# Performance work log

Hardware: AMD Instinct MI355X
Metric: run time of the kernel (lower is better)

Reference implementation:

```python
import jax, jax.numpy as jnp
import numpy as np

NEG_SLOPE = 0.2
CHUNK = 64  # target-node chunk size to bound the [B,c,N,H,D] intermediate


def layer_norm(x, g, b, eps=1e-5):
    mu = jnp.mean(x, axis=-1, keepdims=True)
    var = jnp.mean((x - mu) ** 2, axis=-1, keepdims=True)
    return (x - mu) / jnp.sqrt(var + eps) * g + b


def gatv2_dense(x, Wl, bl, Wr, br, att, bias):
    """GATv2 (PyG semantics, concat=True) on a fully-connected graph with self-loops.
    x: [B,N,Fin]; att: [H,D]. Returns [B,N,H*D].
    e_ij = att_h . leaky_relu(xl_j + xr_i); softmax over sources j; out_i = sum_j a_ij xl_j.
    """
    B, N, _ = x.shape
    H, D = att.shape
    xl = (x @ Wl + bl).reshape(B, N, H, D)  # source-side (lin_l)
    xr = (x @ Wr + br).reshape(B, N, H, D)  # target-side (lin_r)
    nc = N // CHUNK
    xr_ch = jnp.moveaxis(xr.reshape(B, nc, CHUNK, H, D), 1, 0)  # [nc,B,c,H,D]

    @jax.checkpoint
    def per_chunk(xr_c):  # xr_c: [B,c,H,D]
        z = jax.nn.leaky_relu(xr_c[:, :, None] + xl[:, None], NEG_SLOPE)  # [B,c,N,H,D]
        e = jnp.einsum('bcjhd,hd->bcjh', z, att)
        a = jax.nn.softmax(e, axis=2)  # softmax over sources j
        return jnp.einsum('bcjh,bjhd->bchd', a, xl)

    out = jax.lax.map(per_chunk, xr_ch)  # [nc,B,c,H,D]
    return jnp.moveaxis(out, 0, 1).reshape(B, N, H * D) + bias


def setup_inputs() -> dict:
    key = jax.random.key(0)
    ks = jax.random.split(key, 12)
    B, N, Fin, Hd, H, Do = 4, 2048, 32, 32, 4, 32
    f32 = jnp.float32

    def glorot(k, shape, fan_in):
        return jax.random.normal(k, shape, f32) * (1.0 / np.sqrt(fan_in))

    return {
        'x': jax.random.normal(ks[0], (B, N, Fin), f32),
        'embedding': jax.random.normal(ks[1], (N, Hd), f32),
        # layer 1: in=Fin, heads=H, head dim=Hd
        'Wl1': glorot(ks[2], (Fin, H * Hd), Fin), 'bl1': jnp.zeros((H * Hd,), f32),
        'Wr1': glorot(ks[3], (Fin, H * Hd), Fin), 'br1': jnp.zeros((H * Hd,), f32),
        'att1': glorot(ks[4], (H, Hd), Hd), 'bias1': jnp.zeros((H * Hd,), f32),
        'ln1_g': jnp.ones((H * Hd,), f32), 'ln1_b': jnp.zeros((H * Hd,), f32),
        # layer 2: in=H*Hd, heads=H, head dim=Do
        'Wl2': glorot(ks[5], (H * Hd, H * Do), H * Hd), 'bl2': jnp.zeros((H * Do,), f32),
        'Wr2': glorot(ks[6], (H * Hd, H * Do), H * Hd), 'br2': jnp.zeros((H * Do,), f32),
        'att2': glorot(ks[7], (H, Do), Do), 'bias2': jnp.zeros((H * Do,), f32),
        'ln2_g': jnp.ones((H * Do,), f32), 'ln2_b': jnp.zeros((H * Do,), f32),
    }


def reference(x, embedding, Wl1, bl1, Wr1, br1, att1, bias1, ln1_g, ln1_b,
              Wl2, bl2, Wr2, br2, att2, bias2, ln2_g, ln2_b):
    # AdaptiveAdjacency: cosine-similarity gram matrix. Its values are generically
    # all nonzero, so adj[b].nonzero() yields a fully-connected edge list including
    # self-loops; only the connectivity (dense) is consumed downstream.
    ne = embedding / jnp.linalg.norm(embedding, axis=1, keepdims=True)
    adj = ne @ ne.T  # [N,N]; connectivity only (dense), values unused by GATv2
    del adj

    h = layer_norm(gatv2_dense(x, Wl1, bl1, Wr1, br1, att1, bias1), ln1_g, ln1_b)
    h = jax.nn.relu(h)
    # dropout(p=0.3) is identity in eval mode
    out = layer_norm(gatv2_dense(h, Wl2, bl2, Wr2, br2, att2, bias2), ln2_g, ln2_b)
    return out
```

## Files before the change

kernel.cpp:

```cpp
#include <hip/hip_runtime.h>
#include <math.h>

#define LOG2E 1.4426950408889634f

#if __has_builtin(__builtin_amdgcn_exp2f)
#define EXP2(x) __builtin_amdgcn_exp2f(x)
#else
#define EXP2(x) exp2f(x)
#endif

constexpr int B_ = 4, N_ = 2048, H_ = 4, D_ = 32, HD_ = 128;
constexpr int BH_ = B_ * H_;
constexpr int ROWS_ = BH_ * N_;
constexpr size_t M_ = (size_t)ROWS_ * D_;

typedef float v4f __attribute__((ext_vector_type(4)));
typedef _Float16 h2 __attribute__((ext_vector_type(2)));

static __device__ __forceinline__ h2 habs2(h2 z) {
    unsigned int t = __builtin_bit_cast(unsigned int, z) & 0x7FFF7FFFu;
    return __builtin_bit_cast(h2, t);
}
static __device__ __forceinline__ h2 hadd2u(unsigned int a, unsigned int b) {
    return __builtin_bit_cast(h2, a) + __builtin_bit_cast(h2, b);
}
static __device__ __forceinline__ h2 u2h(unsigned int a) {
    return __builtin_bit_cast(h2, a);
}

__global__ __launch_bounds__(256) void k_linear(
    const float* __restrict__ x,
    const float* __restrict__ Wl, const float* __restrict__ bl,
    const float* __restrict__ Wr, const float* __restrict__ br,
    float* __restrict__ xl, unsigned short* __restrict__ xlh,
    unsigned short* __restrict__ xrh, unsigned int* __restrict__ xlpT, int K)
{
    __shared__ __align__(16) float xs[32 * 128];
    const int tid = threadIdx.x;
    const int r0 = blockIdx.x * 32;
    const float4* src = (const float4*)(x + (size_t)r0 * K);
    float4* dst = (float4*)xs;
    for (int idx = tid; idx < 8 * K; idx += 256) dst[idx] = src[idx];
    __syncthreads();

    const int c  = tid & 127;
    const int rg = tid >> 7;
    float accl[16], accr[16];
    const float blv = bl[c], brv = br[c];
    #pragma unroll
    for (int r = 0; r < 16; r++) { accl[r] = blv; accr[r] = brv; }
    #pragma unroll 8
    for (int k = 0; k < K; k++) {
        const float wl = Wl[k * HD_ + c];
        const float wr = Wr[k * HD_ + c];
        #pragma unroll
        for (int r = 0; r < 16; r++) {
            const float xv = xs[(rg * 16 + r) * K + k];
            accl[r] = fmaf(xv, wl, accl[r]);
            accr[r] = fmaf(xv, wr, accr[r]);
        }
    }
    const int h = c >> 5, d = c & 31;
    #pragma unroll
    for (int r = 0; r < 16; r++) {
        const int row = r0 + rg * 16 + r;
        const int b = row >> 11, n = row & (N_ - 1);
        const size_t o = (((size_t)(b * H_ + h)) * N_ + n) * D_ + d;
        xl[o] = accl[r];
        xlh[o] = __builtin_bit_cast(unsigned short, (_Float16)accl[r]);
        xrh[o] = __builtin_bit_cast(unsigned short, (_Float16)accr[r]);
    }
    #pragma unroll
    for (int r = 0; r < 16; r += 2) {
        const int row = r0 + rg * 16 + r;
        const int b = row >> 11, n = row & (N_ - 1);
        h2 pr;
        pr.x = (_Float16)accl[r];
        pr.y = (_Float16)accl[r + 1];
        const size_t o = (((size_t)(b * H_ + h)) * (N_ / 2) + (n >> 1)) * D_ + d;
        xlpT[o] = __builtin_bit_cast(unsigned int, pr);
    }
}

__global__ __launch_bounds__(256) void k_u(
    const float* __restrict__ xl, const float* __restrict__ att,
    float* __restrict__ u)
{
    const int idx = blockIdx.x * 256 + threadIdx.x;
    const int h = (idx / N_) & (H_ - 1);
    const float4* a4 = (const float4*)(att + h * D_);
    const float4* l4 = (const float4*)(xl + (size_t)idx * D_);
    float su = 0.f;
    #pragma unroll
    for (int q = 0; q < 8; q++) {
        const float4 a = a4[q], lv = l4[q];
        su += a.x * lv.x + a.y * lv.y + a.z * lv.z + a.w * lv.w;
    }
    u[idx] = 0.6f * LOG2E * su;
}

__global__ __launch_bounds__(512) void k_bound(
    const unsigned int* __restrict__ xlh, const unsigned int* __restrict__ xrh,
    const float* __restrict__ u, const float* __restrict__ att,
    float* __restrict__ bound, unsigned int* __restrict__ tch)
{
    __shared__ float redA[16][33];
    __shared__ float redB[16][33];
    __shared__ float clv[32];
    __shared__ float tca[32];
    __shared__ float redu[512];
    const int bh = blockIdx.x, h = bh & (H_ - 1), t = threadIdx.x;

    if (bh < H_ && t < 16) {
        h2 v;
        v.x = (_Float16)(att[bh * D_ + 2 * t]     * (0.4f * LOG2E));
        v.y = (_Float16)(att[bh * D_ + 2 * t + 1] * (0.4f * LOG2E));
        tch[bh * 16 + t] = __builtin_bit_cast(unsigned int, v);
    }
    if (t < 16) {
        _Float16 a = (_Float16)(att[h * D_ + 2 * t]     * (0.4f * LOG2E));
        _Float16 b = (_Float16)(att[h * D_ + 2 * t + 1] * (0.4f * LOG2E));
        tca[2 * t]     = fabsf((float)a);
        tca[2 * t + 1] = fabsf((float)b);
    }
    const unsigned int* xb = xlh + (size_t)bh * N_ * 16;
    const int p = t & 15, rg = t >> 4;
    float m0 = 0.f, m1 = 0.f;
    for (int r = rg; r < N_; r += 32) {
        h2 z = __builtin_bit_cast(h2, xb[r * 16 + p] & 0x7FFF7FFFu);
        m0 = fmaxf(m0, (float)z.x);
        m1 = fmaxf(m1, (float)z.y);
    }
    redA[p][rg] = m0; redB[p][rg] = m1;
    const float* ub = u + (size_t)bh * N_;
    float um = -1e30f;
    for (int r = t; r < N_; r += 512) um = fmaxf(um, ub[r]);
    redu[t] = um;
    __syncthreads();
    if (t < 16) {
        float a = 0.f, b = 0.f;
        for (int g = 0; g < 32; g++) { a = fmaxf(a, redA[t][g]); b = fmaxf(b, redB[t][g]); }
        clv[2 * t] = a; clv[2 * t + 1] = b;
    }
    for (int s = 256; s > 0; s >>= 1) {
        if (t < s) redu[t] = fmaxf(redu[t], redu[t + s]);
        __syncthreads();
    }
    const float umax = redu[0];
    const unsigned int* xrb = xrh + (size_t)bh * N_ * 16;
    for (int r = t; r < N_; r += 512) {
        float s = 0.f;
        #pragma unroll
        for (int k = 0; k < 16; k++) {
            h2 z = __builtin_bit_cast(h2, xrb[r * 16 + k] & 0x7FFF7FFFu);
            s += tca[2 * k] * (clv[2 * k] + (float)z.x)
               + tca[2 * k + 1] * (clv[2 * k + 1] + (float)z.y);
        }
        bound[bh * N_ + r] = umax + s + 0.25f;
    }
}

__global__ __launch_bounds__(256) void k_attn(
    const unsigned int* __restrict__ xlh,
    const unsigned int* __restrict__ xlpT,
    const unsigned int* __restrict__ xrh,
    const float* __restrict__ u, const float* __restrict__ bound,
    const unsigned int* __restrict__ tch,
    float* __restrict__ P, float* __restrict__ lb, int jlen)
{
    const int tid = threadIdx.x, lane = tid & 63, wid = tid >> 6;
    const int t128 = blockIdx.x & 127, part = blockIdx.x >> 7;
    const int bh = t128 >> 3;
    const int h  = bh & (H_ - 1);
    const int row = bh * N_ + (t128 & 7) * 256 + wid * 64 + lane;

    h2 tc[16];
    #pragma unroll
    for (int k = 0; k < 16; k++) tc[k] = u2h(tch[h * 16 + k]);

    unsigned int xrp[16];
    {
        const uint4* s = (const uint4*)(xrh + (size_t)row * 16);
        const uint4 a = s[0], b = s[1], c = s[2], d = s[3];
        xrp[0]=a.x; xrp[1]=a.y; xrp[2]=a.z; xrp[3]=a.w;
        xrp[4]=b.x; xrp[5]=b.y; xrp[6]=b.z; xrp[7]=b.w;
        xrp[8]=c.x; xrp[9]=c.y; xrp[10]=c.z; xrp[11]=c.w;
        xrp[12]=d.x; xrp[13]=d.y; xrp[14]=d.z; xrp[15]=d.w;
    }
    const float negb = -bound[row];

    float l = 0.f;
    float o[32];
    #pragma unroll
    for (int k = 0; k < 32; k++) o[k] = 0.f;

    const unsigned int* xlh_b = xlh + (size_t)bh * N_ * 16;
    const unsigned int* xlt_b = xlpT + (size_t)bh * (N_ / 2) * 32;
    const float* u_b = u + (size_t)bh * N_;

    const int jpb = (part * jlen) >> 1, jpe = jpb + (jlen >> 1);
    for (int jp = jpb; jp < jpe; jp++) {
        const unsigned int* w0 = xlh_b + (size_t)(2 * jp) * 16;
        const unsigned int* w1 = w0 + 16;
        float e0 = u_b[2 * jp]     + negb;
        float f0 = 0.f, e1 = u_b[2 * jp + 1] + negb, f1 = 0.f;
        #pragma unroll
        for (int k = 0; k < 16; k += 2) {
            e0 = __builtin_amdgcn_fdot2(habs2(hadd2u(w0[k],     xrp[k])),     tc[k],     e0, false);
            f0 = __builtin_amdgcn_fdot2(habs2(hadd2u(w0[k + 1], xrp[k + 1])), tc[k + 1], f0, false);
            e1 = __builtin_amdgcn_fdot2(habs2(hadd2u(w1[k],     xrp[k])),     tc[k],     e1, false);
            f1 = __builtin_amdgcn_fdot2(habs2(hadd2u(w1[k + 1], xrp[k + 1])), tc[k + 1], f1, false);
        }
        const float p0 = EXP2(e0 + f0);
        const float p1 = EXP2(e1 + f1);
        const h2 p01 = __builtin_bit_cast(h2, __builtin_amdgcn_cvt_pkrtz(p0, p1));
        h2 ones; ones.x = (_Float16)1.f; ones.y = (_Float16)1.f;
        l = __builtin_amdgcn_fdot2(p01, ones, l, false);
        const unsigned int* vp = xlt_b + (size_t)jp * 32;
        #pragma unroll
        for (int d = 0; d < 32; d++)
            o[d] = __builtin_amdgcn_fdot2(p01, u2h(vp[d]), o[d], false);
    }

    float* Pp = P + (size_t)part * M_ + (size_t)row * D_;
    #pragma unroll
    for (int k = 0; k < 8; k++) {
        v4f w;
        w.x = o[4*k]; w.y = o[4*k+1]; w.z = o[4*k+2]; w.w = o[4*k+3];
        ((v4f*)Pp)[k] = w;
    }
    lb[part * ROWS_ + row] = l;
}

template <int JS>
__global__ __launch_bounds__(256) void k_combine(
    const float* __restrict__ P, const float* __restrict__ lb,
    float* __restrict__ ao)
{
    const int idx = blockIdx.x * 256 + threadIdx.x;
    const int row = idx >> 5;
    float L = 0.f;
    #pragma unroll
    for (int s = 0; s < JS; s++) L += lb[s * ROWS_ + row];
    float acc = 0.f;
    #pragma unroll
    for (int s = 0; s < JS; s++) acc += P[(size_t)s * M_ + idx];
    ao[idx] = acc / L;
}

__global__ __launch_bounds__(64) void k_ln(
    const float* __restrict__ ain, const float* __restrict__ bias,
    const float* __restrict__ g, const float* __restrict__ bta,
    float* __restrict__ outp, int do_relu)
{
    const int row = blockIdx.x;
    const int b = row >> 11, n = row & (N_ - 1);
    const int t = threadIdx.x;
    const int c0 = t, c1 = t + 64;
    const size_t i0 = (((size_t)(b * H_ + (c0 >> 5))) * N_ + n) * D_ + (c0 & 31);
    const size_t i1 = (((size_t)(b * H_ + (c1 >> 5))) * N_ + n) * D_ + (c1 & 31);
    const float x0 = ain[i0] + bias[c0];
    const float x1 = ain[i1] + bias[c1];
    float s = x0 + x1;
    #pragma unroll
    for (int w = 1; w < 64; w <<= 1) s += __shfl_xor(s, w);
    const float mu = s * (1.f / 128.f);
    const float d0 = x0 - mu, d1 = x1 - mu;
    float q = d0 * d0 + d1 * d1;
    #pragma unroll
    for (int w = 1; w < 64; w <<= 1) q += __shfl_xor(q, w);
    const float rstd = rsqrtf(q * (1.f / 128.f) + 1e-5f);
    float y0 = d0 * rstd * g[c0] + bta[c0];
    float y1 = d1 * rstd * g[c1] + bta[c1];
    if (do_relu) { y0 = fmaxf(y0, 0.f); y1 = fmaxf(y1, 0.f); }
    outp[(size_t)row * HD_ + c0] = y0;
    outp[(size_t)row * HD_ + c1] = y1;
}

extern "C" void kernel_launch(void* const* d_in, const int* in_sizes, int n_in,
                              void* d_out, int out_size, void* d_ws, size_t ws_size,
                              hipStream_t stream) {
    const float* x    = (const float*)d_in[0];
    const float* Wl1  = (const float*)d_in[2];
    const float* bl1  = (const float*)d_in[3];
    const float* Wr1  = (const float*)d_in[4];
    const float* br1  = (const float*)d_in[5];
    const float* att1 = (const float*)d_in[6];
    const float* bias1= (const float*)d_in[7];
    const float* ln1g = (const float*)d_in[8];
    const float* ln1b = (const float*)d_in[9];
    const float* Wl2  = (const float*)d_in[10];
    const float* bl2  = (const float*)d_in[11];
    const float* Wr2  = (const float*)d_in[12];
    const float* br2  = (const float*)d_in[13];
    const float* att2 = (const float*)d_in[14];
    const float* bias2= (const float*)d_in[15];
    const float* ln2g = (const float*)d_in[16];
    const float* ln2b = (const float*)d_in[17];

    float* ws = (float*)d_ws;
    float* xl = ws;
    unsigned short* xlh = (unsigned short*)(xl + M_);
    unsigned short* xrh = xlh + M_;
    unsigned int* xlpT = (unsigned int*)(xrh + M_);
    float* u     = xl + (size_t)(2.5 * M_);
    float* bound = u + ROWS_;
    unsigned int* tch = (unsigned int*)(bound + ROWS_);

    int js = 1;
    for (int cand = 8; cand >= 1; cand >>= 1) {
        const size_t need = ((size_t)(2.5 * M_) + 2 * ROWS_ + 64
                             + (size_t)cand * (M_ + ROWS_)) * sizeof(float);
        if (ws_size >= need) { js = cand; break; }
    }
    const int jlen = N_ / js;

    float* P  = (float*)(tch + 64);
    float* lb = P + (size_t)js * M_;
    float* h  = P;
    float* ao = xl;
    float* outf = (float*)d_out;

    const int BN = B_ * N_;
    k_linear<<<BN / 32, 256, 0, stream>>>(x, Wl1, bl1, Wr1, br1, xl, xlh, xrh, xlpT, 32);
    k_u<<<ROWS_ / 256, 256, 0, stream>>>(xl, att1, u);
    k_bound<<<BH_, 512, 0, stream>>>((const unsigned int*)xlh, (const unsigned int*)xrh,
                                     u, att1, bound, tch);
    k_attn<<<128 * js, 256, 0, stream>>>((const unsigned int*)xlh, xlpT,
                                         (const unsigned int*)xrh, u, bound, tch, P, lb, jlen);
    if      (js == 8)  k_combine<8><<<(ROWS_ * D_) / 256, 256, 0, stream>>>(P, lb, ao);
    else if (js == 4)  k_combine<4><<<(ROWS_ * D_) / 256, 256, 0, stream>>>(P, lb, ao);
    else if (js == 2)  k_combine<2><<<(ROWS_ * D_) / 256, 256, 0, stream>>>(P, lb, ao);
    else               k_combine<1><<<(ROWS_ * D_) / 256, 256, 0, stream>>>(P, lb, ao);
    k_ln<<<BN, 64, 0, stream>>>(ao, bias1, ln1g, ln1b, h, 1);
    k_linear<<<BN / 32, 256, 0, stream>>>(h, Wl2, bl2, Wr2, br2, xl, xlh, xrh, xlpT, 128);
    k_u<<<ROWS_ / 256, 256, 0, stream>>>(xl, att2, u);
    k_bound<<<BH_, 512, 0, stream>>>((const unsigned int*)xlh, (const unsigned int*)xrh,
                                     u, att2, bound, tch);
    k_attn<<<128 * js, 256, 0, stream>>>((const unsigned int*)xlh, xlpT,
                                         (const unsigned int*)xrh, u, bound, tch, P, lb, jlen);
    if      (js == 8)  k_combine<8><<<(ROWS_ * D_) / 256, 256, 0, stream>>>(P, lb, ao);
    else if (js == 4)  k_combine<4><<<(ROWS_ * D_) / 256, 256, 0, stream>>>(P, lb, ao);
    else if (js == 2)  k_combine<2><<<(ROWS_ * D_) / 256, 256, 0, stream>>>(P, lb, ao);
    else               k_combine<1><<<(ROWS_ * D_) / 256, 256, 0, stream>>>(P, lb, ao);
    k_ln<<<BN, 64, 0, stream>>>(ao, bias2, ln2g, ln2b, outf, 0);
}
```

Measured before the change: 498.3 us.

## Split each attention row across two lanes and fuse combine with layernorm

The attention kernel now assigns each target row to a pair of lanes, each handling half of the head dimension. Partial logits are summed with a lane shuffle, and loads are vectorised as uint4. This halves per-thread registers and doubles the grid, aiming for higher occupancy and latency hiding, at the cost of redundant exp work across the pair and an extra shuffle. The split-combine kernel is also fused into the layernorm kernel, removing one launch and an intermediate buffer round trip, though the workspace requirement grows.

```diff
diff --git a/kernel.cpp b/kernel.cpp
--- a/kernel.cpp
+++ b/kernel.cpp
@@ -169,30 +169,30 @@
     float* __restrict__ P, float* __restrict__ lb, int jlen)
 {
     const int tid = threadIdx.x, lane = tid & 63, wid = tid >> 6;
-    const int t128 = blockIdx.x & 127, part = blockIdx.x >> 7;
-    const int bh = t128 >> 3;
+    const int dh = lane & 1, r = lane >> 1;
+    const int t256 = blockIdx.x & 255, part = blockIdx.x >> 8;
+    const int bh = t256 >> 4;
+    const int i  = (t256 & 15) * 128 + wid * 32 + r;
     const int h  = bh & (H_ - 1);
-    const int row = bh * N_ + (t128 & 7) * 256 + wid * 64 + lane;
-
-    h2 tc[16];
-    #pragma unroll
-    for (int k = 0; k < 16; k++) tc[k] = u2h(tch[h * 16 + k]);
-
-    unsigned int xrp[16];
+    const int row = bh * N_ + i;
+
+    h2 tc[8];
+    #pragma unroll
+    for (int k = 0; k < 8; k++) tc[k] = u2h(tch[h * 16 + dh * 8 + k]);
+
+    unsigned int xrp[8];
     {
-        const uint4* s = (const uint4*)(xrh + (size_t)row * 16);
-        const uint4 a = s[0], b = s[1], c = s[2], d = s[3];
+        const uint4* s = (const uint4*)(xrh + (size_t)row * 16 + dh * 8);
+        const uint4 a = s[0], b = s[1];
         xrp[0]=a.x; xrp[1]=a.y; xrp[2]=a.z; xrp[3]=a.w;
         xrp[4]=b.x; xrp[5]=b.y; xrp[6]=b.z; xrp[7]=b.w;
-        xrp[8]=c.x; xrp[9]=c.y; xrp[10]=c.z; xrp[11]=c.w;
-        xrp[12]=d.x; xrp[13]=d.y; xrp[14]=d.z; xrp[15]=d.w;
     }
     const float negb = -bound[row];
 
     float l = 0.f;
-    float o[32];
-    #pragma unroll
-    for (int k = 0; k < 32; k++) o[k] = 0.f;
+    float o[16];
+    #pragma unroll
+    for (int k = 0; k < 16; k++) o[k] = 0.f;
 
     const unsigned int* xlh_b = xlh + (size_t)bh * N_ * 16;
     const unsigned int* xlt_b = xlpT + (size_t)bh * (N_ / 2) * 32;
@@ -200,67 +200,89 @@
 
     const int jpb = (part * jlen) >> 1, jpe = jpb + (jlen >> 1);
     for (int jp = jpb; jp < jpe; jp++) {
-        const unsigned int* w0 = xlh_b + (size_t)(2 * jp) * 16;
-        const unsigned int* w1 = w0 + 16;
-        float e0 = u_b[2 * jp]     + negb;
-        float f0 = 0.f, e1 = u_b[2 * jp + 1] + negb, f1 = 0.f;
-        #pragma unroll
-        for (int k = 0; k < 16; k += 2) {
-            e0 = __builtin_amdgcn_fdot2(habs2(hadd2u(w0[k],     xrp[k])),     tc[k],     e0, false);
-            f0 = __builtin_amdgcn_fdot2(habs2(hadd2u(w0[k + 1], xrp[k + 1])), tc[k + 1], f0, false);
-            e1 = __builtin_amdgcn_fdot2(habs2(hadd2u(w1[k],     xrp[k])),     tc[k],     e1, false);
-            f1 = __builtin_amdgcn_fdot2(habs2(hadd2u(w1[k + 1], xrp[k + 1])), tc[k + 1], f1, false);
-        }
-        const float p0 = EXP2(e0 + f0);
-        const float p1 = EXP2(e1 + f1);
+        const uint4* wp0 = (const uint4*)(xlh_b + (size_t)(2 * jp) * 16 + dh * 8);
+        const uint4* wp1 = (const uint4*)(xlh_b + (size_t)(2 * jp) * 16 + 16 + dh * 8);
+        const uint4 wa0 = wp0[0], wb0 = wp0[1];
+        const uint4 wa1 = wp1[0], wb1 = wp1[1];
+        float e0 = 0.f, f0 = 0.f, e1 = 0.f, f1 = 0.f;
+        e0 = __builtin_amdgcn_fdot2(habs2(hadd2u(wa0.x, xrp[0])), tc[0], e0, false);
+        f0 = __builtin_amdgcn_fdot2(habs2(hadd2u(wa0.y, xrp[1])), tc[1], f0, false);
+        e0 = __builtin_amdgcn_fdot2(habs2(hadd2u(wa0.z, xrp[2])), tc[2], e0, false);
+        f0 = __builtin_amdgcn_fdot2(habs2(hadd2u(wa0.w, xrp[3])), tc[3], f0, false);
+        e0 = __builtin_amdgcn_fdot2(habs2(hadd2u(wb0.x, xrp[4])), tc[4], e0, false);
+        f0 = __builtin_amdgcn_fdot2(habs2(hadd2u(wb0.y, xrp[5])), tc[5], f0, false);
+        e0 = __builtin_amdgcn_fdot2(habs2(hadd2u(wb0.z, xrp[6])), tc[6], e0, false);
+        f0 = __builtin_amdgcn_fdot2(habs2(hadd2u(wb0.w, xrp[7])), tc[7], f0, false);
+        e1 = __builtin_amdgcn_fdot2(habs2(hadd2u(wa1.x, xrp[0])), tc[0], e1, false);
+        f1 = __builtin_amdgcn_fdot2(habs2(hadd2u(wa1.y, xrp[1])), tc[1], f1, false);
+        e1 = __builtin_amdgcn_fdot2(habs2(hadd2u(wa1.z, xrp[2])), tc[2], e1, false);
+        f1 = __builtin_amdgcn_fdot2(habs2(hadd2u(wa1.w, xrp[3])), tc[3], f1, false);
+        e1 = __builtin_amdgcn_fdot2(habs2(hadd2u(wb1.x, xrp[4])), tc[4], e1, false);
+        f1 = __builtin_amdgcn_fdot2(habs2(hadd2u(wb1.y, xrp[5])), tc[5], f1, false);
+        e1 = __builtin_amdgcn_fdot2(habs2(hadd2u(wb1.z, xrp[6])), tc[6], e1, false);
+        f1 = __builtin_amdgcn_fdot2(habs2(hadd2u(wb1.w, xrp[7])), tc[7], f1, false);
+        float ep0 = e0 + f0;
+        float ep1 = e1 + f1;
+        ep0 += __shfl_xor(ep0, 1);
+        ep1 += __shfl_xor(ep1, 1);
+        const float p0 = EXP2(ep0 + (u_b[2 * jp]     + negb));
+        const float p1 = EXP2(ep1 + (u_b[2 * jp + 1] + negb));
         const h2 p01 = __builtin_bit_cast(h2, __builtin_amdgcn_cvt_pkrtz(p0, p1));
         h2 ones; ones.x = (_Float16)1.f; ones.y = (_Float16)1.f;
         l = __builtin_amdgcn_fdot2(p01, ones, l, false);
-        const unsigned int* vp = xlt_b + (size_t)jp * 32;
-        #pragma unroll
-        for (int d = 0; d < 32; d++)
-            o[d] = __builtin_amdgcn_fdot2(p01, u2h(vp[d]), o[d], false);
-    }
-
-    float* Pp = P + (size_t)part * M_ + (size_t)row * D_;
-    #pragma unroll
-    for (int k = 0; k < 8; k++) {
+        const uint4* vp = (const uint4*)(xlt_b + (size_t)jp * 32 + dh * 16);
+        const uint4 v0 = vp[0], v1 = vp[1], v2 = vp[2], v3 = vp[3];
+        o[0]  = __builtin_amdgcn_fdot2(p01, u2h(v0.x), o[0],  false);
+        o[1]  = __builtin_amdgcn_fdot2(p01, u2h(v0.y), o[1],  false);
+        o[2]  = __builtin_amdgcn_fdot2(p01, u2h(v0.z), o[2],  false);
+        o[3]  = __builtin_amdgcn_fdot2(p01, u2h(v0.w), o[3],  false);
+        o[4]  = __builtin_amdgcn_fdot2(p01, u2h(v1.x), o[4],  false);
+        o[5]  = __builtin_amdgcn_fdot2(p01, u2h(v1.y), o[5],  false);
+        o[6]  = __builtin_amdgcn_fdot2(p01, u2h(v1.z), o[6],  false);
+        o[7]  = __builtin_amdgcn_fdot2(p01, u2h(v1.w), o[7],  false);
+        o[8]  = __builtin_amdgcn_fdot2(p01, u2h(v2.x), o[8],  false);
+        o[9]  = __builtin_amdgcn_fdot2(p01, u2h(v2.y), o[9],  false);
+        o[10] = __builtin_amdgcn_fdot2(p01, u2h(v2.z), o[10], false);
+        o[11] = __builtin_amdgcn_fdot2(p01, u2h(v2.w), o[11], false);
+        o[12] = __builtin_amdgcn_fdot2(p01, u2h(v3.x), o[12], false);
+        o[13] = __builtin_amdgcn_fdot2(p01, u2h(v3.y), o[13], false);
+        o[14] = __builtin_amdgcn_fdot2(p01, u2h(v3.z), o[14], false);
+        o[15] = __builtin_amdgcn_fdot2(p01, u2h(v3.w), o[15], false);
+    }
+
+    float* Pp = P + (size_t)part * M_ + (size_t)row * D_ + dh * 16;
+    #pragma unroll
+    for (int k = 0; k < 4; k++) {
         v4f w;
         w.x = o[4*k]; w.y = o[4*k+1]; w.z = o[4*k+2]; w.w = o[4*k+3];
         ((v4f*)Pp)[k] = w;
     }
-    lb[part * ROWS_ + row] = l;
+    if (dh == 0) lb[part * ROWS_ + row] = l;
 }
 
 template <int JS>
-__global__ __launch_bounds__(256) void k_combine(
+__global__ __launch_bounds__(64) void k_comb_ln(
     const float* __restrict__ P, const float* __restrict__ lb,
-    float* __restrict__ ao)
-{
-    const int idx = blockIdx.x * 256 + threadIdx.x;
-    const int row = idx >> 5;
-    float L = 0.f;
-    #pragma unroll
-    for (int s = 0; s < JS; s++) L += lb[s * ROWS_ + row];
-    float acc = 0.f;
-    #pragma unroll
-    for (int s = 0; s < JS; s++) acc += P[(size_t)s * M_ + idx];
-    ao[idx] = acc / L;
-}
-
-__global__ __launch_bounds__(64) void k_ln(
-    const float* __restrict__ ain, const float* __restrict__ bias,
-    const float* __restrict__ g, const float* __restrict__ bta,
-    float* __restrict__ outp, int do_relu)
+    const float* __restrict__ bias, const float* __restrict__ g,
+    const float* __restrict__ bta, float* __restrict__ outp, int do_relu)
 {
     const int row = blockIdx.x;
     const int b = row >> 11, n = row & (N_ - 1);
     const int t = threadIdx.x;
     const int c0 = t, c1 = t + 64;
-    const size_t i0 = (((size_t)(b * H_ + (c0 >> 5))) * N_ + n) * D_ + (c0 & 31);
-    const size_t i1 = (((size_t)(b * H_ + (c1 >> 5))) * N_ + n) * D_ + (c1 & 31);
-    const float x0 = ain[i0] + bias[c0];
-    const float x1 = ain[i1] + bias[c1];
+    const int bh0 = b * H_ + (c0 >> 5), bh1 = b * H_ + (c1 >> 5);
+    const size_t i0 = ((size_t)bh0 * N_ + n) * D_ + (c0 & 31);
+    const size_t i1 = ((size_t)bh1 * N_ + n) * D_ + (c1 & 31);
+    float a0 = 0.f, a1 = 0.f, L0 = 0.f, L1 = 0.f;
+    #pragma unroll
+    for (int s = 0; s < JS; s++) {
+        a0 += P[(size_t)s * M_ + i0];
+        a1 += P[(size_t)s * M_ + i1];
+        L0 += lb[s * ROWS_ + bh0 * N_ + n];
+        L1 += lb[s * ROWS_ + bh1 * N_ + n];
+    }
+    const float x0 = a0 / L0 + bias[c0];
+    const float x1 = a1 / L1 + bias[c1];
     float s = x0 + x1;
     #pragma unroll
     for (int w = 1; w < 64; w <<= 1) s += __shfl_xor(s, w);
@@ -309,7 +331,7 @@
 
     int js = 1;
     for (int cand = 8; cand >= 1; cand >>= 1) {
-        const size_t need = ((size_t)(2.5 * M_) + 2 * ROWS_ + 64
+        const size_t need = ((size_t)(3.5 * M_) + 2 * ROWS_ + 64
                              + (size_t)cand * (M_ + ROWS_)) * sizeof(float);
         if (ws_size >= need) { js = cand; break; }
     }
@@ -317,8 +339,7 @@
 
     float* P  = (float*)(tch + 64);
     float* lb = P + (size_t)js * M_;
-    float* h  = P;
-    float* ao = xl;
+    float* h  = lb + (size_t)js * ROWS_;
     float* outf = (float*)d_out;
 
     const int BN = B_ * N_;
@@ -326,22 +347,20 @@
     k_u<<<ROWS_ / 256, 256, 0, stream>>>(xl, att1, u);
     k_bound<<<BH_, 512, 0, stream>>>((const unsigned int*)xlh, (const unsigned int*)xrh,
                                      u, att1, bound, tch);
-    k_attn<<<128 * js, 256, 0, stream>>>((const unsigned int*)xlh, xlpT,
+    k_attn<<<256 * js, 256, 0, stream>>>((const unsigned int*)xlh, xlpT,
                                          (const unsigned int*)xrh, u, bound, tch, P, lb, jlen);
-    if      (js == 8)  k_combine<8><<<(ROWS_ * D_) / 256, 256, 0, stream>>>(P, lb, ao);
-    else if (js == 4)  k_combine<4><<<(ROWS_ * D_) / 256, 256, 0, stream>>>(P, lb, ao);
-    else if (js == 2)  k_combine<2><<<(ROWS_ * D_) / 256, 256, 0, stream>>>(P, lb, ao);
-    else               k_combine<1><<<(ROWS_ * D_) / 256, 256, 0, stream>>>(P, lb, ao);
-    k_ln<<<BN, 64, 0, stream>>>(ao, bias1, ln1g, ln1b, h, 1);
+    if      (js == 8) k_comb_ln<8><<<BN, 64, 0, stream>>>(P, lb, bias1, ln1g, ln1b, h, 1);
+    else if (js == 4) k_comb_ln<4><<<BN, 64, 0, stream>>>(P, lb, bias1, ln1g, ln1b, h, 1);
+    else if (js == 2) k_comb_ln<2><<<BN, 64, 0, stream>>>(P, lb, bias1, ln1g, ln1b, h, 1);
+    else              k_comb_ln<1><<<BN, 64, 0, stream>>>(P, lb, bias1, ln1g, ln1b, h, 1);
     k_linear<<<BN / 32, 256, 0, stream>>>(h, Wl2, bl2, Wr2, br2, xl, xlh, xrh, xlpT, 128);
     k_u<<<ROWS_ / 256, 256, 0, stream>>>(xl, att2, u);
     k_bound<<<BH_, 512, 0, stream>>>((const unsigned int*)xlh, (const unsigned int*)xrh,
                                      u, att2, bound, tch);
-    k_attn<<<128 * js, 256, 0, stream>>>((const unsigned int*)xlh, xlpT,
+    k_attn<<<256 * js, 256, 0, stream>>>((const unsigned int*)xlh, xlpT,
                                          (const unsigned int*)xrh, u, bound, tch, P, lb, jlen);
-    if      (js == 8)  k_combine<8><<<(ROWS_ * D_) / 256, 256, 0, stream>>>(P, lb, ao);
-    else if (js == 4)  k_combine<4><<<(ROWS_ * D_) / 256, 256, 0, stream>>>(P, lb, ao);
-    else if (js == 2)  k_combine<2><<<(ROWS_ * D_) / 256, 256, 0, stream>>>(P, lb, ao);
-    else               k_combine<1><<<(ROWS_ * D_) / 256, 256, 0, stream>>>(P, lb, ao);
-    k_ln<<<BN, 64, 0, stream>>>(ao, bias2, ln2g, ln2b, outf, 0);
-}
+    if      (js == 8) k_comb_ln<8><<<BN, 64, 0, stream>>>(P, lb, bias2, ln2g, ln2b, outf, 0);
+    else if (js == 4) k_comb_ln<4><<<BN, 64, 0, stream>>>(P, lb, bias2, ln2g, ln2b, outf, 0);
+    else if (js == 2) k_comb_ln<2><<<BN, 64, 0, stream>>>(P, lb, bias2, ln2g, ln2b, outf, 0);
+    else              k_comb_ln<1><<<BN, 64, 0, stream>>>(P, lb, bias2, ln2g, ln2b, outf, 0);
+}
```

Result: slower. 665.9 us (+33.6%).
